# Kernel optimization log

Hardware: AMD Instinct MI355X
Metric: run time of the kernel (lower is better)

## Reference

```python
import jax, jax.numpy as jnp
import numpy as np

IN_FEATURES = 1024
OUT_FEATURES = 4096
HARMONICS = 32
TOKENS = 16384


def setup_inputs() -> dict:
    key = jax.random.key(0)
    k_x, k_basis, k_phase = jax.random.split(key, 3)
    x = jax.random.normal(k_x, (TOKENS, IN_FEATURES), dtype=jnp.float32)
    basis = jax.random.normal(k_basis, (HARMONICS, IN_FEATURES), dtype=jnp.float32)
    # F.normalize(basis, p=2, dim=1)
    basis = basis / jnp.linalg.norm(basis, axis=1, keepdims=True)
    two_pi = 2.0 * np.pi
    phase = jax.random.normal(k_phase, (OUT_FEATURES, HARMONICS), dtype=jnp.float32) * two_pi
    amp = jnp.ones((OUT_FEATURES, HARMONICS), dtype=jnp.float32) / HARMONICS
    return {"x": x, "basis": basis, "phase": phase, "amp": amp}


def reference(x, basis, phase, amp):
    # resonance = F.linear(x, basis): [T, H]
    resonance = jnp.einsum("ti,hi->th", x, basis)
    # wave is complex(resonance, 0); resonator = amp * exp(i*phase).
    # real((wave * resonator).sum(-1)) == resonance @ (amp*cos(phase))^T since wave.imag == 0.
    w_real = amp * jnp.cos(phase)  # [O, H]
    return jnp.einsum("th,oh->to", resonance, w_real)
```

## Files before the change

kernel.cpp:

```cpp
#include <hip/hip_runtime.h>

#define T_TOK 16384
#define IN_F  1024
#define OUT_F 4096
#define NH    32

__global__ __launch_bounds__(256) void wreal_kernel(
    const float* __restrict__ phase, const float* __restrict__ amp,
    float* __restrict__ w_t)
{
    int idx = blockIdx.x * 256 + threadIdx.x;
    int o = idx & (OUT_F - 1);
    int h = idx >> 12;
    float p = phase[o * NH + h];
    float a = amp[o * NH + h];
    w_t[h * OUT_F + o] = a * cosf(p);
}

#define G1_TT 64
#define G1_KC 128
#define G1_S  132

__global__ __launch_bounds__(256) void resonance_kernel(
    const float* __restrict__ x,
    const float* __restrict__ basis,
    float* __restrict__ res_t)
{
    __shared__ float xs[G1_TT * G1_S];
    __shared__ float bs[NH * G1_S];

    const int tid = threadIdx.x;
    const int t0  = blockIdx.x * G1_TT;
    const int ty  = tid >> 4;
    const int tx  = tid & 15;

    float acc[4][2] = {};

    for (int i0 = 0; i0 < IN_F; i0 += G1_KC) {
        #pragma unroll
        for (int it = 0; it < 8; ++it) {
            int lin = it * 256 + tid;
            int r = lin >> 5, c = lin & 31;
            float4 v = *(const float4*)(x + (size_t)(t0 + r) * IN_F + i0 + 4 * c);
            *(float4*)(xs + r * G1_S + 4 * c) = v;
        }
        #pragma unroll
        for (int it = 0; it < 4; ++it) {
            int lin = it * 256 + tid;
            int r = lin >> 5, c = lin & 31;
            float4 v = *(const float4*)(basis + (size_t)r * IN_F + i0 + 4 * c);
            *(float4*)(bs + r * G1_S + 4 * c) = v;
        }
        __syncthreads();

        #pragma unroll 4
        for (int i = 0; i < G1_KC; i += 4) {
            float4 xa[4], bb[2];
            #pragma unroll
            for (int k = 0; k < 4; ++k)
                xa[k] = *(const float4*)(xs + (4 * ty + k) * G1_S + i);
            #pragma unroll
            for (int j = 0; j < 2; ++j)
                bb[j] = *(const float4*)(bs + (tx + 16 * j) * G1_S + i);
            #pragma unroll
            for (int k = 0; k < 4; ++k) {
                #pragma unroll
                for (int j = 0; j < 2; ++j) {
                    acc[k][j] += xa[k].x * bb[j].x;
                    acc[k][j] += xa[k].y * bb[j].y;
                    acc[k][j] += xa[k].z * bb[j].z;
                    acc[k][j] += xa[k].w * bb[j].w;
                }
            }
        }
        __syncthreads();
    }

    #pragma unroll
    for (int k = 0; k < 4; ++k)
        #pragma unroll
        for (int j = 0; j < 2; ++j)
            res_t[(size_t)(tx + 16 * j) * T_TOK + t0 + 4 * ty + k] = acc[k][j];
}

#define G2_TT 64
#define G2_OT 128
#define RS_S  68
#define WT_S  132

__global__ __launch_bounds__(256) void holo_out_kernel(
    const float* __restrict__ res_t,
    const float* __restrict__ w_t,
    float* __restrict__ out)
{
    __shared__ float rs[NH * RS_S];
    __shared__ float wl[NH * WT_S];

    const int tid = threadIdx.x;
    const int o0  = blockIdx.x * G2_OT;
    const int t0  = blockIdx.y * G2_TT;
    const int ty  = tid >> 4;
    const int tx  = tid & 15;

    #pragma unroll
    for (int it = 0; it < 2; ++it) {
        int lin = it * 256 + tid;
        int r = lin >> 4, c = lin & 15;
        float4 v = *(const float4*)(res_t + (size_t)r * T_TOK + t0 + 4 * c);
        *(float4*)(rs + r * RS_S + 4 * c) = v;
    }
    #pragma unroll
    for (int it = 0; it < 4; ++it) {
        int lin = it * 256 + tid;
        int r = lin >> 5, c = lin & 31;
        float4 v = *(const float4*)(w_t + (size_t)r * OUT_F + o0 + 4 * c);
        *(float4*)(wl + r * WT_S + 4 * c) = v;
    }
    __syncthreads();

    float acc[4][8] = {};
    #pragma unroll
    for (int h = 0; h < NH; ++h) {
        float4 rt = *(const float4*)(rs + h * RS_S + 4 * ty);
        float4 wa = *(const float4*)(wl + h * WT_S + 4 * tx);
        float4 wb = *(const float4*)(wl + h * WT_S + 64 + 4 * tx);
        float r4[4] = {rt.x, rt.y, rt.z, rt.w};
        float w8[8] = {wa.x, wa.y, wa.z, wa.w, wb.x, wb.y, wb.z, wb.w};
        #pragma unroll
        for (int k = 0; k < 4; ++k)
            #pragma unroll
            for (int j = 0; j < 8; ++j)
                acc[k][j] += r4[k] * w8[j];
    }

    #pragma unroll
    for (int k = 0; k < 4; ++k) {
        float* po = out + (size_t)(t0 + 4 * ty + k) * OUT_F + o0;
        *(float4*)(po + 4 * tx)      = make_float4(acc[k][0], acc[k][1], acc[k][2], acc[k][3]);
        *(float4*)(po + 64 + 4 * tx) = make_float4(acc[k][4], acc[k][5], acc[k][6], acc[k][7]);
    }
}

extern "C" void kernel_launch(void* const* d_in, const int* in_sizes, int n_in,
                              void* d_out, int out_size, void* d_ws, size_t ws_size,
                              hipStream_t stream)
{
    const float* x     = (const float*)d_in[0];
    const float* basis = (const float*)d_in[1];
    const float* phase = (const float*)d_in[2];
    const float* amp   = (const float*)d_in[3];
    float* out = (float*)d_out;

    float* res_t = (float*)d_ws;
    float* w_t   = res_t + (size_t)NH * T_TOK;

    wreal_kernel<<<dim3((OUT_F * NH) / 256), dim3(256), 0, stream>>>(phase, amp, w_t);
    resonance_kernel<<<dim3(T_TOK / G1_TT), dim3(256), 0, stream>>>(x, basis, res_t);
    holo_out_kernel<<<dim3(OUT_F / G2_OT, T_TOK / G2_TT), dim3(256), 0, stream>>>(res_t, w_t, out);
}
```

Measured before the change: 353.2 us.

## Rewrite resonance GEMM as register split-K with shuffle reduce; enlarge output tiles

The resonance kernel drops shared-memory staging. Each thread holds 32 harmonic accumulators for two tokens over a strided slice of the input, prefetches x into registers and reads basis straight from global/L2. A butterfly of shuffle-xor steps then reduces and transposes the partial sums across the 16 lanes. The output kernel's tile grows from 64x128 to 128x256, so each thread computes an 8x16 micro-tile, which raises FMA-per-LDS reuse but costs many more registers and risks lower occupancy.

New measurement: 380.2 us. +7.6%, slower.

```diff
diff --git a/kernel.cpp b/kernel.cpp
--- a/kernel.cpp
+++ b/kernel.cpp
@@ -17,78 +17,84 @@
     w_t[h * OUT_F + o] = a * cosf(p);
 }
 
-#define G1_TT 64
-#define G1_KC 128
-#define G1_S  132
+#define K2_TT 32
 
-__global__ __launch_bounds__(256) void resonance_kernel(
+__global__ __launch_bounds__(256, 2) void resonance_kernel(
     const float* __restrict__ x,
     const float* __restrict__ basis,
     float* __restrict__ res_t)
 {
-    __shared__ float xs[G1_TT * G1_S];
-    __shared__ float bs[NH * G1_S];
-
     const int tid = threadIdx.x;
-    const int t0  = blockIdx.x * G1_TT;
     const int ty  = tid >> 4;
     const int tx  = tid & 15;
+    const size_t ta = (size_t)blockIdx.x * K2_TT + 2 * ty;
 
-    float acc[4][2] = {};
+    const float* xa = x + ta * IN_F + 4 * tx;
+    const float* xb = xa + IN_F;
+    const float* bp = basis + 4 * tx;
 
-    for (int i0 = 0; i0 < IN_F; i0 += G1_KC) {
-        #pragma unroll
-        for (int it = 0; it < 8; ++it) {
-            int lin = it * 256 + tid;
-            int r = lin >> 5, c = lin & 31;
-            float4 v = *(const float4*)(x + (size_t)(t0 + r) * IN_F + i0 + 4 * c);
-            *(float4*)(xs + r * G1_S + 4 * c) = v;
+    float v0[NH] = {};
+    float v1[NH] = {};
+
+    float4 pa = *(const float4*)(xa);
+    float4 pb = *(const float4*)(xb);
+
+    for (int i0 = 0; i0 < IN_F; i0 += 64) {
+        float4 ca = pa, cb = pb;
+        if (i0 + 64 < IN_F) {
+            pa = *(const float4*)(xa + i0 + 64);
+            pb = *(const float4*)(xb + i0 + 64);
         }
         #pragma unroll
-        for (int it = 0; it < 4; ++it) {
-            int lin = it * 256 + tid;
-            int r = lin >> 5, c = lin & 31;
-            float4 v = *(const float4*)(basis + (size_t)r * IN_F + i0 + 4 * c);
-            *(float4*)(bs + r * G1_S + 4 * c) = v;
-        }
-        __syncthreads();
-
-        #pragma unroll 4
-        for (int i = 0; i < G1_KC; i += 4) {
-            float4 xa[4], bb[2];
+        for (int hg = 0; hg < 4; ++hg) {
+            float4 bv[8];
             #pragma unroll
-            for (int k = 0; k < 4; ++k)
-                xa[k] = *(const float4*)(xs + (4 * ty + k) * G1_S + i);
+            for (int h = 0; h < 8; ++h)
+                bv[h] = *(const float4*)(bp + (size_t)(8 * hg + h) * IN_F + i0);
             #pragma unroll
-            for (int j = 0; j < 2; ++j)
-                bb[j] = *(const float4*)(bs + (tx + 16 * j) * G1_S + i);
-            #pragma unroll
-            for (int k = 0; k < 4; ++k) {
-                #pragma unroll
-                for (int j = 0; j < 2; ++j) {
-                    acc[k][j] += xa[k].x * bb[j].x;
-                    acc[k][j] += xa[k].y * bb[j].y;
-                    acc[k][j] += xa[k].z * bb[j].z;
-                    acc[k][j] += xa[k].w * bb[j].w;
-                }
+            for (int h = 0; h < 8; ++h) {
+                const int hh = 8 * hg + h;
+                v0[hh] += ca.x * bv[h].x;
+                v0[hh] += ca.y * bv[h].y;
+                v0[hh] += ca.z * bv[h].z;
+                v0[hh] += ca.w * bv[h].w;
+                v1[hh] += cb.x * bv[h].x;
+                v1[hh] += cb.y * bv[h].y;
+                v1[hh] += cb.z * bv[h].z;
+                v1[hh] += cb.w * bv[h].w;
             }
         }
-        __syncthreads();
     }
 
     #pragma unroll
-    for (int k = 0; k < 4; ++k)
+    for (int s = 0; s < 4; ++s) {
+        const int m = 1 << s;
+        const int half = 16 >> s;
+        const bool up = (tx & m) != 0;
         #pragma unroll
-        for (int j = 0; j < 2; ++j)
-            res_t[(size_t)(tx + 16 * j) * T_TOK + t0 + 4 * ty + k] = acc[k][j];
+        for (int h = 0; h < half; ++h) {
+            float a0 = v0[h], b0 = v0[h + half];
+            float k0 = up ? b0 : a0;
+            float g0 = up ? a0 : b0;
+            v0[h] = k0 + __shfl_xor(g0, m, 64);
+            float a1 = v1[h], b1 = v1[h + half];
+            float k1 = up ? b1 : a1;
+            float g1 = up ? a1 : b1;
+            v1[h] = k1 + __shfl_xor(g1, m, 64);
+        }
+    }
+
+    const int h0 = ((tx & 1) << 4) | ((tx & 2) << 2) | (tx & 4) | ((tx & 8) >> 2);
+    *(float2*)(res_t + (size_t)h0 * T_TOK + ta)       = make_float2(v0[0], v1[0]);
+    *(float2*)(res_t + (size_t)(h0 + 1) * T_TOK + ta) = make_float2(v0[1], v1[1]);
 }
 
-#define G2_TT 64
-#define G2_OT 128
-#define RS_S  68
-#define WT_S  132
+#define G2_TT 128
+#define G2_OT 256
+#define RS_S  132
+#define WT_S  260
 
-__global__ __launch_bounds__(256) void holo_out_kernel(
+__global__ __launch_bounds__(256, 2) void holo_out_kernel(
     const float* __restrict__ res_t,
     const float* __restrict__ w_t,
     float* __restrict__ out)
@@ -103,41 +109,47 @@
     const int tx  = tid & 15;
 
     #pragma unroll
-    for (int it = 0; it < 2; ++it) {
+    for (int it = 0; it < 4; ++it) {
         int lin = it * 256 + tid;
-        int r = lin >> 4, c = lin & 15;
+        int r = lin >> 5, c = lin & 31;
         float4 v = *(const float4*)(res_t + (size_t)r * T_TOK + t0 + 4 * c);
         *(float4*)(rs + r * RS_S + 4 * c) = v;
     }
     #pragma unroll
-    for (int it = 0; it < 4; ++it) {
+    for (int it = 0; it < 8; ++it) {
         int lin = it * 256 + tid;
-        int r = lin >> 5, c = lin & 31;
+        int r = lin >> 6, c = lin & 63;
         float4 v = *(const float4*)(w_t + (size_t)r * OUT_F + o0 + 4 * c);
         *(float4*)(wl + r * WT_S + 4 * c) = v;
     }
     __syncthreads();
 
-    float acc[4][8] = {};
+    float acc[8][16] = {};
     #pragma unroll
     for (int h = 0; h < NH; ++h) {
-        float4 rt = *(const float4*)(rs + h * RS_S + 4 * ty);
-        float4 wa = *(const float4*)(wl + h * WT_S + 4 * tx);
-        float4 wb = *(const float4*)(wl + h * WT_S + 64 + 4 * tx);
-        float r4[4] = {rt.x, rt.y, rt.z, rt.w};
-        float w8[8] = {wa.x, wa.y, wa.z, wa.w, wb.x, wb.y, wb.z, wb.w};
+        float4 r0 = *(const float4*)(rs + h * RS_S + 8 * ty);
+        float4 r1 = *(const float4*)(rs + h * RS_S + 8 * ty + 4);
+        float4 w0 = *(const float4*)(wl + h * WT_S + 4 * tx);
+        float4 w1 = *(const float4*)(wl + h * WT_S + 64 + 4 * tx);
+        float4 w2 = *(const float4*)(wl + h * WT_S + 128 + 4 * tx);
+        float4 w3 = *(const float4*)(wl + h * WT_S + 192 + 4 * tx);
+        float r8[8]   = {r0.x, r0.y, r0.z, r0.w, r1.x, r1.y, r1.z, r1.w};
+        float w16[16] = {w0.x, w0.y, w0.z, w0.w, w1.x, w1.y, w1.z, w1.w,
+                         w2.x, w2.y, w2.z, w2.w, w3.x, w3.y, w3.z, w3.w};
         #pragma unroll
-        for (int k = 0; k < 4; ++k)
+        for (int k = 0; k < 8; ++k)
             #pragma unroll
-            for (int j = 0; j < 8; ++j)
-                acc[k][j] += r4[k] * w8[j];
+            for (int j = 0; j < 16; ++j)
+                acc[k][j] += r8[k] * w16[j];
     }
 
     #pragma unroll
-    for (int k = 0; k < 4; ++k) {
-        float* po = out + (size_t)(t0 + 4 * ty + k) * OUT_F + o0;
-        *(float4*)(po + 4 * tx)      = make_float4(acc[k][0], acc[k][1], acc[k][2], acc[k][3]);
-        *(float4*)(po + 64 + 4 * tx) = make_float4(acc[k][4], acc[k][5], acc[k][6], acc[k][7]);
+    for (int k = 0; k < 8; ++k) {
+        float* po = out + (size_t)(t0 + 8 * ty + k) * OUT_F + o0;
+        *(float4*)(po + 4 * tx)       = make_float4(acc[k][0],  acc[k][1],  acc[k][2],  acc[k][3]);
+        *(float4*)(po + 64 + 4 * tx)  = make_float4(acc[k][4],  acc[k][5],  acc[k][6],  acc[k][7]);
+        *(float4*)(po + 128 + 4 * tx) = make_float4(acc[k][8],  acc[k][9],  acc[k][10], acc[k][11]);
+        *(float4*)(po + 192 + 4 * tx) = make_float4(acc[k][12], acc[k][13], acc[k][14], acc[k][15]);
     }
 }
 
@@ -155,6 +167,6 @@
     float* w_t   = res_t + (size_t)NH * T_TOK;
 
     wreal_kernel<<<dim3((OUT_F * NH) / 256), dim3(256), 0, stream>>>(phase, amp, w_t);
-    resonance_kernel<<<dim3(T_TOK / G1_TT), dim3(256), 0, stream>>>(x, basis, res_t);
+    resonance_kernel<<<dim3(T_TOK / K2_TT), dim3(256), 0, stream>>>(x, basis, res_t);
     holo_out_kernel<<<dim3(OUT_F / G2_OT, T_TOK / G2_TT), dim3(256), 0, stream>>>(res_t, w_t, out);
 }
```

## Fuse resonance and output projection into one kernel with double-buffered weight tiles

Applied to the files above, without the earlier changes.

Merges the resonance GEMM and the output GEMM into one kernel per 64-token tile. The resonance tile stays in shared memory instead of round-tripping through a global workspace, and one kernel launch goes away. Each block then loops over all 32 output-column chunks, double-buffering the cos-weight tile with register prefetch. The trade-off is a grid of only 256 blocks of 4 waves each for the store-heavy output phase, so occupancy and latency hiding for the large output write may suffer.

Result: slower. 402.4 us (+13.9%).

```diff
diff --git a/kernel.cpp b/kernel.cpp
--- a/kernel.cpp
+++ b/kernel.cpp
@@ -17,51 +17,57 @@
     w_t[h * OUT_F + o] = a * cosf(p);
 }
 
-#define G1_TT 64
-#define G1_KC 128
-#define G1_S  132
+#define F_TT  64
+#define KC    128
+#define XS_S  132
+#define RS_S  68
+#define WT_S  132
+#define NOC   (OUT_F / 128)
 
-__global__ __launch_bounds__(256) void resonance_kernel(
+__global__ __launch_bounds__(256) void fused_kernel(
     const float* __restrict__ x,
     const float* __restrict__ basis,
-    float* __restrict__ res_t)
+    const float* __restrict__ w_t,
+    float* __restrict__ out)
 {
-    __shared__ float xs[G1_TT * G1_S];
-    __shared__ float bs[NH * G1_S];
+    __shared__ float rs[NH * RS_S];
+    __shared__ float sbuf[F_TT * XS_S + NH * XS_S];
 
     const int tid = threadIdx.x;
-    const int t0  = blockIdx.x * G1_TT;
+    const int t0  = blockIdx.x * F_TT;
     const int ty  = tid >> 4;
     const int tx  = tid & 15;
 
+    float* xs = sbuf;
+    float* bs = sbuf + F_TT * XS_S;
+
     float acc[4][2] = {};
-
-    for (int i0 = 0; i0 < IN_F; i0 += G1_KC) {
+    for (int i0 = 0; i0 < IN_F; i0 += KC) {
         #pragma unroll
         for (int it = 0; it < 8; ++it) {
             int lin = it * 256 + tid;
             int r = lin >> 5, c = lin & 31;
             float4 v = *(const float4*)(x + (size_t)(t0 + r) * IN_F + i0 + 4 * c);
-            *(float4*)(xs + r * G1_S + 4 * c) = v;
+            *(float4*)(xs + r * XS_S + 4 * c) = v;
         }
         #pragma unroll
         for (int it = 0; it < 4; ++it) {
             int lin = it * 256 + tid;
             int r = lin >> 5, c = lin & 31;
             float4 v = *(const float4*)(basis + (size_t)r * IN_F + i0 + 4 * c);
-            *(float4*)(bs + r * G1_S + 4 * c) = v;
+            *(float4*)(bs + r * XS_S + 4 * c) = v;
         }
         __syncthreads();
 
         #pragma unroll 4
-        for (int i = 0; i < G1_KC; i += 4) {
+        for (int i = 0; i < KC; i += 4) {
             float4 xa[4], bb[2];
             #pragma unroll
             for (int k = 0; k < 4; ++k)
-                xa[k] = *(const float4*)(xs + (4 * ty + k) * G1_S + i);
+                xa[k] = *(const float4*)(xs + (4 * ty + k) * XS_S + i);
             #pragma unroll
             for (int j = 0; j < 2; ++j)
-                bb[j] = *(const float4*)(bs + (tx + 16 * j) * G1_S + i);
+                bb[j] = *(const float4*)(bs + (tx + 16 * j) * XS_S + i);
             #pragma unroll
             for (int k = 0; k < 4; ++k) {
                 #pragma unroll
@@ -77,67 +83,77 @@
     }
 
     #pragma unroll
-    for (int k = 0; k < 4; ++k)
-        #pragma unroll
-        for (int j = 0; j < 2; ++j)
-            res_t[(size_t)(tx + 16 * j) * T_TOK + t0 + 4 * ty + k] = acc[k][j];
-}
+    for (int j = 0; j < 2; ++j)
+        *(float4*)(rs + (tx + 16 * j) * RS_S + 4 * ty) =
+            make_float4(acc[0][j], acc[1][j], acc[2][j], acc[3][j]);
 
-#define G2_TT 64
-#define G2_OT 128
-#define RS_S  68
-#define WT_S  132
-
-__global__ __launch_bounds__(256) void holo_out_kernel(
-    const float* __restrict__ res_t,
-    const float* __restrict__ w_t,
-    float* __restrict__ out)
-{
-    __shared__ float rs[NH * RS_S];
-    __shared__ float wl[NH * WT_S];
-
-    const int tid = threadIdx.x;
-    const int o0  = blockIdx.x * G2_OT;
-    const int t0  = blockIdx.y * G2_TT;
-    const int ty  = tid >> 4;
-    const int tx  = tid & 15;
+    float* wl = sbuf;
+    float4 nw[4];
 
     #pragma unroll
-    for (int it = 0; it < 2; ++it) {
+    for (int it = 0; it < 4; ++it) {
         int lin = it * 256 + tid;
-        int r = lin >> 4, c = lin & 15;
-        float4 v = *(const float4*)(res_t + (size_t)r * T_TOK + t0 + 4 * c);
-        *(float4*)(rs + r * RS_S + 4 * c) = v;
+        int r = lin >> 5, c = lin & 31;
+        nw[it] = *(const float4*)(w_t + (size_t)r * OUT_F + 4 * c);
     }
     #pragma unroll
     for (int it = 0; it < 4; ++it) {
         int lin = it * 256 + tid;
         int r = lin >> 5, c = lin & 31;
-        float4 v = *(const float4*)(w_t + (size_t)r * OUT_F + o0 + 4 * c);
-        *(float4*)(wl + r * WT_S + 4 * c) = v;
+        *(float4*)(wl + r * WT_S + 4 * c) = nw[it];
+    }
+    #pragma unroll
+    for (int it = 0; it < 4; ++it) {
+        int lin = it * 256 + tid;
+        int r = lin >> 5, c = lin & 31;
+        nw[it] = *(const float4*)(w_t + (size_t)r * OUT_F + 128 + 4 * c);
     }
     __syncthreads();
 
-    float acc[4][8] = {};
-    #pragma unroll
-    for (int h = 0; h < NH; ++h) {
-        float4 rt = *(const float4*)(rs + h * RS_S + 4 * ty);
-        float4 wa = *(const float4*)(wl + h * WT_S + 4 * tx);
-        float4 wb = *(const float4*)(wl + h * WT_S + 64 + 4 * tx);
-        float r4[4] = {rt.x, rt.y, rt.z, rt.w};
-        float w8[8] = {wa.x, wa.y, wa.z, wa.w, wb.x, wb.y, wb.z, wb.w};
+    for (int oc = 0; oc < NOC; ++oc) {
+        const float* wcur = wl + (oc & 1) * (NH * WT_S);
+        const int o0 = oc * 128;
+
+        float acc2[4][8] = {};
         #pragma unroll
-        for (int k = 0; k < 4; ++k)
+        for (int h = 0; h < NH; ++h) {
+            float4 rt = *(const float4*)(rs + h * RS_S + 4 * ty);
+            float4 wa = *(const float4*)(wcur + h * WT_S + 4 * tx);
+            float4 wb = *(const float4*)(wcur + h * WT_S + 64 + 4 * tx);
+            float r4[4] = {rt.x, rt.y, rt.z, rt.w};
+            float w8[8] = {wa.x, wa.y, wa.z, wa.w, wb.x, wb.y, wb.z, wb.w};
             #pragma unroll
-            for (int j = 0; j < 8; ++j)
-                acc[k][j] += r4[k] * w8[j];
-    }
+            for (int k = 0; k < 4; ++k)
+                #pragma unroll
+                for (int j = 0; j < 8; ++j)
+                    acc2[k][j] += r4[k] * w8[j];
+        }
 
-    #pragma unroll
-    for (int k = 0; k < 4; ++k) {
-        float* po = out + (size_t)(t0 + 4 * ty + k) * OUT_F + o0;
-        *(float4*)(po + 4 * tx)      = make_float4(acc[k][0], acc[k][1], acc[k][2], acc[k][3]);
-        *(float4*)(po + 64 + 4 * tx) = make_float4(acc[k][4], acc[k][5], acc[k][6], acc[k][7]);
+        #pragma unroll
+        for (int k = 0; k < 4; ++k) {
+            float* po = out + (size_t)(t0 + 4 * ty + k) * OUT_F + o0;
+            *(float4*)(po + 4 * tx)      = make_float4(acc2[k][0], acc2[k][1], acc2[k][2], acc2[k][3]);
+            *(float4*)(po + 64 + 4 * tx) = make_float4(acc2[k][4], acc2[k][5], acc2[k][6], acc2[k][7]);
+        }
+
+        if (oc + 1 < NOC) {
+            float* wnext = wl + ((oc + 1) & 1) * (NH * WT_S);
+            #pragma unroll
+            for (int it = 0; it < 4; ++it) {
+                int lin = it * 256 + tid;
+                int r = lin >> 5, c = lin & 31;
+                *(float4*)(wnext + r * WT_S + 4 * c) = nw[it];
+            }
+            if (oc + 2 < NOC) {
+                #pragma unroll
+                for (int it = 0; it < 4; ++it) {
+                    int lin = it * 256 + tid;
+                    int r = lin >> 5, c = lin & 31;
+                    nw[it] = *(const float4*)(w_t + (size_t)r * OUT_F + (oc + 2) * 128 + 4 * c);
+                }
+            }
+            __syncthreads();
+        }
     }
 }
 
@@ -151,10 +167,8 @@
     const float* amp   = (const float*)d_in[3];
     float* out = (float*)d_out;
 
-    float* res_t = (float*)d_ws;
-    float* w_t   = res_t + (size_t)NH * T_TOK;
+    float* w_t = (float*)d_ws;
 
     wreal_kernel<<<dim3((OUT_F * NH) / 256), dim3(256), 0, stream>>>(phase, amp, w_t);
-    resonance_kernel<<<dim3(T_TOK / G1_TT), dim3(256), 0, stream>>>(x, basis, res_t);
-    holo_out_kernel<<<dim3(OUT_F / G2_OT, T_TOK / G2_TT), dim3(256), 0, stream>>>(res_t, w_t, out);
+    fused_kernel<<<dim3(T_TOK / F_TT), dim3(256), 0, stream>>>(x, basis, w_t, out);
 }
```
